# Kernel tuning notes

Measured on AMD Instinct MI355X. Metric: run time of the kernel, lower is better.

## Reference

```python
import jax, jax.numpy as jnp
import numpy as np

N = 100_000      # atom_count
E = 6_400_000    # number of (directed) edges, avg degree 64
BOX = 100.0      # simulation box edge length


def setup_inputs() -> dict:
    key = jax.random.key(0)
    k1, k2, k3 = jax.random.split(key, 3)
    pos = jax.random.uniform(k1, (N, 3), dtype=jnp.float32) * BOX
    src = jax.random.randint(k2, (E,), 0, N, dtype=jnp.int32)
    # offset in [1, N) guarantees dst != src (no zero-distance self edges)
    off = jax.random.randint(k3, (E,), 1, N, dtype=jnp.int32)
    dst = ((src + off) % N).astype(jnp.int32)
    edge_index = jnp.stack([src, dst], axis=0)  # [2, E]
    sigma = jnp.asarray(0.3, dtype=jnp.float32)
    epsilon = jnp.asarray(1.0, dtype=jnp.float32)
    return {"pos": pos, "sigma": sigma, "epsilon": epsilon, "edge_index": edge_index}


def _total_energy(pos, sigma, epsilon, src, dst):
    # r = edge_attr: per-edge distance, differentiable w.r.t. pos
    d = pos[src] - pos[dst]                      # [E, 3] gather + subtract
    r = jnp.sqrt(jnp.sum(d * d, axis=-1))        # [E]
    sr6 = (sigma / r) ** 6
    # potential_formula: 4*epsilon*((sigma/r)**12 - (sigma/r)**6)
    v_r = 4.0 * epsilon * (sr6 * sr6 - sr6)      # [E]
    return v_r.sum()


def reference(pos, sigma, epsilon, edge_index):
    src, dst = edge_index[0], edge_index[1]
    energy = _total_energy(pos, sigma, epsilon, src, dst)
    # afc: autograd force — grad of summed pair potential w.r.t. positions
    # (per-edge force scattered onto atoms by edge_index; grad does the
    #  gather-compute-scatter in one pass)
    pair_force = jax.grad(_total_energy, argnums=0)(pos, sigma, epsilon, src, dst)
    atom_force = -pair_force / 2.0               # /2: each pair counted twice
    return energy, atom_force
```

## Files before the change

kernel.cpp:

```cpp
#include <hip/hip_runtime.h>


#define ROW_F   307200

#define NB2     16
#define BA2     6400
#define BF2     (BA2 * 3)
#define KCH     16
#define SCG     256
#define SCB     512
#define NWAVES  2048
#define CAP     512

#define NBINS      8
#define BIN_ATOMS  12800
#define BIN_F      (BIN_ATOMS * 3)
#define BLOCK      1024
#define MAXCHUNKS  32

__global__ __launch_bounds__(SCB) void pf_scatter(
    const float* __restrict__ pos,
    float4*      __restrict__ pos4,
    const int*   __restrict__ src,
    const int*   __restrict__ dst,
    unsigned*    __restrict__ buckets,
    unsigned*    __restrict__ cnt,
    int nEdges, int nAtoms)
{
    __shared__ unsigned shcur[(SCB / 64) * NB2];
    const int t = threadIdx.x, lane = t & 63, wv = t >> 6;
    if (t < (SCB / 64) * NB2) shcur[t] = 0;

    for (int i = blockIdx.x * SCB + t; i < nAtoms; i += SCG * SCB)
        pos4[i] = make_float4(pos[3 * i + 0], pos[3 * i + 1], pos[3 * i + 2], 0.f);

    __syncthreads();

    unsigned* mycur = shcur + wv * NB2;
    const int w    = blockIdx.x * (SCB / 64) + wv;
    const int epw  = (nEdges + NWAVES - 1) / NWAVES;
    const int ebeg = w * epw;
    const int eend = min(nEdges, ebeg + epw);

    int  e   = ebeg + lane;
    bool act = e < eend;
    int  s = 0, d = 0;
    if (act) { s = src[e]; d = dst[e]; }

    for (int base = ebeg; base < eend; base += 64) {
        const int  en   = base + 64 + lane;
        const bool actn = en < eend;
        int sn = 0, dn = 0;
        if (actn) { sn = src[en]; dn = dst[en]; }
        if (act) {
            const unsigned su = (unsigned)s, du = (unsigned)d;
            const unsigned sb = su / BA2, db = du / BA2;
            const unsigned recS = ((su - sb * BA2) << 18) | (1u << 17) | du;
            const unsigned recD = ((du - db * BA2) << 18) | su;
            const unsigned is = atomicAdd(&mycur[sb], 1u);
            if (is < CAP) buckets[((size_t)w * NB2 + sb) * CAP + is] = recS;
            const unsigned id = atomicAdd(&mycur[db], 1u);
            if (id < CAP) buckets[((size_t)w * NB2 + db) * CAP + id] = recD;
        }
        act = actn; s = sn; d = dn;
    }
    __syncthreads();
    if (lane < NB2) {
        const unsigned cv = mycur[lane];
        cnt[w * NB2 + lane] = cv < CAP ? cv : CAP;
    }
}

__global__ __launch_bounds__(1024, 1) void pf_accum(
    const float*    __restrict__ pos,
    const float4*   __restrict__ pos4,
    const float*    __restrict__ sigma_p,
    const float*    __restrict__ eps_p,
    const unsigned* __restrict__ buckets,
    const unsigned* __restrict__ cnt,
    float* __restrict__ frep,
    float* __restrict__ erep,
    int nAtoms)
{
    extern __shared__ float sh[];
    float* shp = sh + BF2 + 16;
    const int t = threadIdx.x, lane = t & 63, v = t >> 6;
    const int b = blockIdx.x / KCH;
    const int c = blockIdx.x % KCH;

    for (int j = t; j < (BF2 + 16) / 4; j += 1024)
        ((float4*)sh)[j] = make_float4(0.f, 0.f, 0.f, 0.f);

    const int binStart = b * BA2;
    const int binCnt   = min(BA2, nAtoms - binStart);
    const int nf       = binCnt * 3;
    const float4* gp   = (const float4*)(pos + (size_t)binStart * 3);
    for (int j = t; j < (nf >> 2); j += 1024) ((float4*)shp)[j] = gp[j];
    for (int j = (nf & ~3) + t; j < nf; j += 1024) shp[j] = pos[binStart * 3 + j];
    __syncthreads();

    const float sigma = sigma_p[0], eps = eps_p[0];
    const float sig2 = sigma * sigma;
    const float c12 = 12.f * eps, c4 = 4.f * eps;

    float ev = 0.f;
    const int slot = c * 16 + v;
    for (int k = 0; k < NWAVES / 256; ++k) {
        const int w = slot + (k << 8);
        const int n = cnt[w * NB2 + b];
        const unsigned* seg = buckets + ((size_t)w * NB2 + b) * CAP;
        for (int j = lane; j < n; j += 64) {
            const unsigned rec = seg[j];
            const int   la = rec >> 18;
            const int   o  = rec & 0x1FFFF;
            const float fl = (rec & (1u << 17)) ? 1.f : 0.f;
            const float ax = shp[3 * la + 0];
            const float ay = shp[3 * la + 1];
            const float az = shp[3 * la + 2];
            const float4 po = pos4[o];
            const float dx = ax - po.x, dy = ay - po.y, dz = az - po.z;
            const float r2   = dx * dx + dy * dy + dz * dz;
            const float ir2  = 1.0f / r2;
            const float s2   = sig2 * ir2;
            const float sr6  = s2 * s2 * s2;
            const float sr12 = sr6 * sr6;
            const float fs   = c12 * (2.f * sr12 - sr6) * ir2;
            atomicAdd(&sh[3 * la + 0], fs * dx);
            atomicAdd(&sh[3 * la + 1], fs * dy);
            atomicAdd(&sh[3 * la + 2], fs * dz);
            ev += fl * c4 * (sr12 - sr6);
        }
    }

    #pragma unroll
    for (int off = 32; off > 0; off >>= 1) ev += __shfl_down(ev, off, 64);
    if (lane == 0) sh[BF2 + v] = ev;
    __syncthreads();

    float4* outSeg = (float4*)(frep + (size_t)c * ROW_F + (size_t)b * BF2);
    for (int j = t; j < BF2 / 4; j += 1024) outSeg[j] = ((float4*)sh)[j];

    if (t == 0) {
        float e = 0.f;
        #pragma unroll
        for (int w2 = 0; w2 < 16; ++w2) e += sh[BF2 + w2];
        erep[blockIdx.x] = e;
    }
}

__global__ __launch_bounds__(256) void pairforce_reduce(
    const float* __restrict__ frep,
    const float* __restrict__ erep,
    float* __restrict__ out,
    int n3, int nChunks, int nPart)
{
    const int i = blockIdx.x * 256 + threadIdx.x;
    if (i < n3) {
        float acc = 0.f;
        for (int c = 0; c < nChunks; ++c)
            acc += frep[(size_t)c * ROW_F + i];
        out[1 + i] = acc;
    }
    if (blockIdx.x == gridDim.x - 1) {
        float e = 0.f;
        for (int j = threadIdx.x; j < nPart; j += 256) e += erep[j];
        #pragma unroll
        for (int off = 32; off > 0; off >>= 1) e += __shfl_down(e, off, 64);
        __shared__ float ep[4];
        if ((threadIdx.x & 63) == 0) ep[threadIdx.x >> 6] = e;
        __syncthreads();
        if (threadIdx.x == 0) out[0] = ep[0] + ep[1] + ep[2] + ep[3];
    }
}

__global__ __launch_bounds__(BLOCK, 1) void pairforce_binned(
    const float* __restrict__ pos,
    const float* __restrict__ sigma_p,
    const float* __restrict__ eps_p,
    const int*   __restrict__ src,
    const int*   __restrict__ dst,
    float* __restrict__ frep,
    float* __restrict__ erep,
    int nEdges, int chunkEdges)
{
    extern __shared__ float sh[];
    const int t = threadIdx.x;
    const int b = blockIdx.x % NBINS;
    const int c = blockIdx.x / NBINS;

    for (int j = t; j < (BIN_F + 16) / 4; j += BLOCK)
        ((float4*)sh)[j] = make_float4(0.f, 0.f, 0.f, 0.f);
    __syncthreads();

    const float sigma = sigma_p[0];
    const float eps   = eps_p[0];
    const float sig2  = sigma * sigma;
    const int binStart = b * BIN_ATOMS;

    const int start = c * chunkEdges;
    const int end   = min(start + chunkEdges, nEdges);

    const int4* src4 = (const int4*)src;
    const int4* dst4 = (const int4*)dst;

    float ev = 0.0f;

    for (int i4 = (start >> 2) + t; i4 < (end >> 2); i4 += BLOCK) {
        const int4 s4 = src4[i4];
        const int4 d4 = dst4[i4];
        #pragma unroll
        for (int k = 0; k < 4; ++k) {
            const int s = (k == 0) ? s4.x : (k == 1) ? s4.y : (k == 2) ? s4.z : s4.w;
            const int d = (k == 0) ? d4.x : (k == 1) ? d4.y : (k == 2) ? d4.z : d4.w;
            const unsigned ls = (unsigned)(s - binStart);
            const unsigned ld = (unsigned)(d - binStart);
            const bool hs = ls < BIN_ATOMS;
            const bool hd = ld < BIN_ATOMS;
            if (hs | hd) {
                const float dx = pos[3 * s + 0] - pos[3 * d + 0];
                const float dy = pos[3 * s + 1] - pos[3 * d + 1];
                const float dz = pos[3 * s + 2] - pos[3 * d + 2];
                const float r2     = dx * dx + dy * dy + dz * dz;
                const float inv_r2 = 1.0f / r2;
                const float s2     = sig2 * inv_r2;
                const float sr6    = s2 * s2 * s2;
                const float sr12   = sr6 * sr6;
                const float fs = 12.0f * eps * (2.0f * sr12 - sr6) * inv_r2;
                const float fx = fs * dx;
                const float fy = fs * dy;
                const float fz = fs * dz;
                if (hs) {
                    atomicAdd(&sh[3 * ls + 0],  fx);
                    atomicAdd(&sh[3 * ls + 1],  fy);
                    atomicAdd(&sh[3 * ls + 2],  fz);
                    ev += 4.0f * eps * (sr12 - sr6);
                }
                if (hd) {
                    atomicAdd(&sh[3 * ld + 0], -fx);
                    atomicAdd(&sh[3 * ld + 1], -fy);
                    atomicAdd(&sh[3 * ld + 2], -fz);
                }
            }
        }
    }

    #pragma unroll
    for (int off = 32; off > 0; off >>= 1)
        ev += __shfl_down(ev, off, 64);
    if ((t & 63) == 0) sh[BIN_F + (t >> 6)] = ev;
    __syncthreads();

    float4* outSeg = (float4*)(frep + (size_t)c * ROW_F + (size_t)b * BIN_F);
    for (int j = t; j < BIN_F / 4; j += BLOCK)
        outSeg[j] = ((float4*)sh)[j];

    if (t == 0) {
        float e = 0.f;
        #pragma unroll
        for (int w = 0; w < 16; ++w) e += sh[BIN_F + w];
        erep[blockIdx.x] = e;
    }
}

extern "C" void kernel_launch(void* const* d_in, const int* in_sizes, int n_in,
                              void* d_out, int out_size, void* d_ws, size_t ws_size,
                              hipStream_t stream)
{
    const float* pos     = (const float*)d_in[0];
    const float* sigma_p = (const float*)d_in[1];
    const float* eps_p   = (const float*)d_in[2];
    const int*   edge    = (const int*)d_in[3];

    const int nEdges = in_sizes[3] / 2;
    const int* src = edge;
    const int* dst = edge + nEdges;

    const int n3 = out_size - 1;
    const int nAtoms = n3 / 3;

    size_t off = 0;
    float*    pos4    = (float*)d_ws;                    off += (size_t)(NB2 * BA2) * 16;
    unsigned* buckets = (unsigned*)((char*)d_ws + off);  off += (size_t)NWAVES * NB2 * CAP * 4;
    unsigned* cntp    = (unsigned*)((char*)d_ws + off);  off += (size_t)NWAVES * NB2 * 4;
    float*    frepN   = (float*)((char*)d_ws + off);     off += (size_t)KCH * ROW_F * 4;
    float*    erepN   = (float*)((char*)d_ws + off);     off += 256 * 4;

    if (ws_size >= off && nAtoms <= NB2 * BA2) {
        pf_scatter<<<SCG, SCB, 0, stream>>>(pos, (float4*)pos4, src, dst,
                                            buckets, cntp, nEdges, nAtoms);
        const size_t shb = (size_t)(BF2 + 16 + BF2) * sizeof(float);
        pf_accum<<<NB2 * KCH, 1024, shb, stream>>>(pos, (const float4*)pos4,
                                                   sigma_p, eps_p, buckets, cntp,
                                                   frepN, erepN, nAtoms);
        pairforce_reduce<<<(n3 + 255) / 256, 256, 0, stream>>>(
            frepN, erepN, (float*)d_out, n3, KCH, NB2 * KCH);
        return;
    }

    const size_t rowBytes = (size_t)ROW_F * sizeof(float);
    int nChunks = (int)((ws_size - 4096) / rowBytes);
    if (nChunks > MAXCHUNKS) nChunks = MAXCHUNKS;
    if (nChunks < 1) nChunks = 1;

    const int chunkEdges = (((nEdges + nChunks - 1) / nChunks) + 3) & ~3;

    float* frep = (float*)d_ws;
    float* erep = frep + (size_t)nChunks * ROW_F;

    const size_t shbytes = (size_t)(BIN_F + 16) * sizeof(float);

    const int grid1 = nChunks * NBINS;
    pairforce_binned<<<grid1, BLOCK, shbytes, stream>>>(
        pos, sigma_p, eps_p, src, dst, frep, erep, nEdges, chunkEdges);

    const int grid2 = (n3 + 255) / 256;
    pairforce_reduce<<<grid2, 256, 0, stream>>>(
        frep, erep, (float*)d_out, n3, nChunks, nChunks * NBINS);
}
```

Before: 373.2 us.

## Vectorize edge loads, pair waves per bucket segment, batch gathers in accumulate

The scatter kernel now reads src/dst as int4 and launches twice as many blocks, with two waves sharing each bucket segment's counters. This doubles parallelism while keeping the number of segments the same. The accumulate kernel loads bucket records as uint4 and issues up to eight position gathers before doing any compute, so more memory requests are in flight at once. It assumes each segment holds at most 512 records (two uint4 loads per lane) and now requires the edge count to be a multiple of four.

```diff
diff --git a/kernel.cpp b/kernel.cpp
--- a/kernel.cpp
+++ b/kernel.cpp
@@ -7,9 +7,9 @@
 #define BA2     6400
 #define BF2     (BA2 * 3)
 #define KCH     16
-#define SCG     256
+#define NSEG    2048
+#define SCG     512
 #define SCB     512
-#define NWAVES  2048
 #define CAP     512
 
 #define NBINS      8
@@ -27,47 +27,58 @@
     unsigned*    __restrict__ cnt,
     int nEdges, int nAtoms)
 {
-    __shared__ unsigned shcur[(SCB / 64) * NB2];
+    __shared__ unsigned shcur[4 * NB2];
     const int t = threadIdx.x, lane = t & 63, wv = t >> 6;
-    if (t < (SCB / 64) * NB2) shcur[t] = 0;
+    if (t < 4 * NB2) shcur[t] = 0;
 
     for (int i = blockIdx.x * SCB + t; i < nAtoms; i += SCG * SCB)
         pos4[i] = make_float4(pos[3 * i + 0], pos[3 * i + 1], pos[3 * i + 2], 0.f);
 
     __syncthreads();
 
-    unsigned* mycur = shcur + wv * NB2;
-    const int w    = blockIdx.x * (SCB / 64) + wv;
-    const int epw  = (nEdges + NWAVES - 1) / NWAVES;
-    const int ebeg = w * epw;
+    const int p = blockIdx.x * 8 + wv;
+    const int w = p >> 1;
+    unsigned* mycur = shcur + (wv >> 1) * NB2;
+
+    const int epw  = ((nEdges + 2 * NSEG - 1) / (2 * NSEG) + 3) & ~3;
+    const int ebeg = p * epw;
     const int eend = min(nEdges, ebeg + epw);
-
-    int  e   = ebeg + lane;
-    bool act = e < eend;
-    int  s = 0, d = 0;
-    if (act) { s = src[e]; d = dst[e]; }
-
-    for (int base = ebeg; base < eend; base += 64) {
-        const int  en   = base + 64 + lane;
-        const bool actn = en < eend;
-        int sn = 0, dn = 0;
-        if (actn) { sn = src[en]; dn = dst[en]; }
-        if (act) {
-            const unsigned su = (unsigned)s, du = (unsigned)d;
-            const unsigned sb = su / BA2, db = du / BA2;
-            const unsigned recS = ((su - sb * BA2) << 18) | (1u << 17) | du;
-            const unsigned recD = ((du - db * BA2) << 18) | su;
-            const unsigned is = atomicAdd(&mycur[sb], 1u);
-            if (is < CAP) buckets[((size_t)w * NB2 + sb) * CAP + is] = recS;
-            const unsigned id = atomicAdd(&mycur[db], 1u);
-            if (id < CAP) buckets[((size_t)w * NB2 + db) * CAP + id] = recD;
+    const int i4beg = ebeg >> 2;
+    const int i4end = eend >> 2;
+
+    const int4* src4 = (const int4*)src;
+    const int4* dst4 = (const int4*)dst;
+
+    int4 s4 = make_int4(0, 0, 0, 0), d4 = make_int4(0, 0, 0, 0);
+    {
+        const int i4 = i4beg + lane;
+        if (i4 < i4end) { s4 = src4[i4]; d4 = dst4[i4]; }
+    }
+    for (int base = i4beg; base < i4end; base += 64) {
+        const int  i4n  = base + 64 + lane;
+        const bool actn = i4n < i4end;
+        int4 s4n = make_int4(0, 0, 0, 0), d4n = make_int4(0, 0, 0, 0);
+        if (actn) { s4n = src4[i4n]; d4n = dst4[i4n]; }
+        if (base + lane < i4end) {
+            #pragma unroll
+            for (int k = 0; k < 4; ++k) {
+                const unsigned su = (unsigned)((k == 0) ? s4.x : (k == 1) ? s4.y : (k == 2) ? s4.z : s4.w);
+                const unsigned du = (unsigned)((k == 0) ? d4.x : (k == 1) ? d4.y : (k == 2) ? d4.z : d4.w);
+                const unsigned sb = su / BA2, db = du / BA2;
+                const unsigned recS = ((su - sb * BA2) << 18) | (1u << 17) | du;
+                const unsigned recD = ((du - db * BA2) << 18) | su;
+                const unsigned is = atomicAdd(&mycur[sb], 1u);
+                if (is < CAP) buckets[((size_t)w * NB2 + sb) * CAP + is] = recS;
+                const unsigned id = atomicAdd(&mycur[db], 1u);
+                if (id < CAP) buckets[((size_t)w * NB2 + db) * CAP + id] = recD;
+            }
         }
-        act = actn; s = sn; d = dn;
-    }
-    __syncthreads();
-    if (lane < NB2) {
-        const unsigned cv = mycur[lane];
-        cnt[w * NB2 + lane] = cv < CAP ? cv : CAP;
+        s4 = s4n; d4 = d4n;
+    }
+    __syncthreads();
+    if (t < 4 * NB2) {
+        const unsigned cv = shcur[t];
+        cnt[(blockIdx.x * 4) * NB2 + t] = cv < CAP ? cv : CAP;
     }
 }
 
@@ -105,30 +116,53 @@
 
     float ev = 0.f;
     const int slot = c * 16 + v;
-    for (int k = 0; k < NWAVES / 256; ++k) {
+
+    for (int k = 0; k < NSEG / 256; ++k) {
         const int w = slot + (k << 8);
         const int n = cnt[w * NB2 + b];
-        const unsigned* seg = buckets + ((size_t)w * NB2 + b) * CAP;
-        for (int j = lane; j < n; j += 64) {
-            const unsigned rec = seg[j];
-            const int   la = rec >> 18;
-            const int   o  = rec & 0x1FFFF;
-            const float fl = (rec & (1u << 17)) ? 1.f : 0.f;
+        const uint4* seg4 = (const uint4*)(buckets + ((size_t)w * NB2 + b) * CAP);
+        const int n4 = (n + 3) >> 2;
+
+        uint4 rqA = make_uint4(0u, 0u, 0u, 0u);
+        uint4 rqB = make_uint4(0u, 0u, 0u, 0u);
+        if (lane < n4)      rqA = seg4[lane];
+        if (lane + 64 < n4) rqB = seg4[lane + 64];
+        const int baseA = 4 * lane;
+        const int baseB = 4 * (lane + 64);
+
+        unsigned rr[8];
+        float4   po[8];
+        #pragma unroll
+        for (int e = 0; e < 8; ++e) {
+            const int rb = (e < 4) ? (baseA + e) : (baseB + e - 4);
+            unsigned rec = (e == 0) ? rqA.x : (e == 1) ? rqA.y : (e == 2) ? rqA.z :
+                           (e == 3) ? rqA.w : (e == 4) ? rqB.x : (e == 5) ? rqB.y :
+                           (e == 6) ? rqB.z : rqB.w;
+            rec = (rb < n) ? rec : 0u;
+            rr[e] = rec;
+            po[e] = pos4[rec & 0x1FFFF];
+        }
+        #pragma unroll
+        for (int e = 0; e < 8; ++e) {
+            const int rb = (e < 4) ? (baseA + e) : (baseB + e - 4);
+            const unsigned rec = rr[e];
+            const int la = rec >> 18;
             const float ax = shp[3 * la + 0];
             const float ay = shp[3 * la + 1];
             const float az = shp[3 * la + 2];
-            const float4 po = pos4[o];
-            const float dx = ax - po.x, dy = ay - po.y, dz = az - po.z;
+            const float dx = ax - po[e].x, dy = ay - po[e].y, dz = az - po[e].z;
             const float r2   = dx * dx + dy * dy + dz * dz;
             const float ir2  = 1.0f / r2;
             const float s2   = sig2 * ir2;
             const float sr6  = s2 * s2 * s2;
             const float sr12 = sr6 * sr6;
             const float fs   = c12 * (2.f * sr12 - sr6) * ir2;
-            atomicAdd(&sh[3 * la + 0], fs * dx);
-            atomicAdd(&sh[3 * la + 1], fs * dy);
-            atomicAdd(&sh[3 * la + 2], fs * dz);
-            ev += fl * c4 * (sr12 - sr6);
+            if (rb < n) {
+                atomicAdd(&sh[3 * la + 0], fs * dx);
+                atomicAdd(&sh[3 * la + 1], fs * dy);
+                atomicAdd(&sh[3 * la + 2], fs * dz);
+                ev += (rec & (1u << 17)) ? c4 * (sr12 - sr6) : 0.f;
+            }
         }
     }
 
@@ -280,12 +314,12 @@
 
     size_t off = 0;
     float*    pos4    = (float*)d_ws;                    off += (size_t)(NB2 * BA2) * 16;
-    unsigned* buckets = (unsigned*)((char*)d_ws + off);  off += (size_t)NWAVES * NB2 * CAP * 4;
-    unsigned* cntp    = (unsigned*)((char*)d_ws + off);  off += (size_t)NWAVES * NB2 * 4;
+    unsigned* buckets = (unsigned*)((char*)d_ws + off);  off += (size_t)NSEG * NB2 * CAP * 4;
+    unsigned* cntp    = (unsigned*)((char*)d_ws + off);  off += (size_t)NSEG * NB2 * 4;
     float*    frepN   = (float*)((char*)d_ws + off);     off += (size_t)KCH * ROW_F * 4;
     float*    erepN   = (float*)((char*)d_ws + off);     off += 256 * 4;
 
-    if (ws_size >= off && nAtoms <= NB2 * BA2) {
+    if (ws_size >= off && nAtoms <= NB2 * BA2 && (nEdges & 3) == 0) {
         pf_scatter<<<SCG, SCB, 0, stream>>>(pos, (float4*)pos4, src, dst,
                                             buckets, cntp, nEdges, nAtoms);
         const size_t shb = (size_t)(BF2 + 16 + BF2) * sizeof(float);
```

Result: faster. 342.8 us (-8.2%).
